# Optimization experiments

Hardware: AMD Instinct MI355X
Metric: run time of the kernel (lower is better)

The kernel has to match this reference:

```python
import jax, jax.numpy as jnp
import numpy as np

H_LSTM = 80          # span-encoder LSTM hidden
SPAN_DIM = 4 * H_LSTM  # 320
ADU_DIM = 256        # han_out_size
HEADS = 3
HAN_HID = 256
CTX_DIM = 200


def lstm(x, W_ih, W_hh, b, reverse=False):
    # x: [T, B, In] -> hidden states [T, B, H]; torch gate order i,f,g,o
    H = W_hh.shape[1]
    B = x.shape[1]

    def step(carry, xt):
        h, c = carry
        z = xt @ W_ih.T + h @ W_hh.T + b
        i, f, g, o = jnp.split(z, 4, axis=-1)
        c = jax.nn.sigmoid(f) * c + jax.nn.sigmoid(i) * jnp.tanh(g)
        h = jax.nn.sigmoid(o) * jnp.tanh(c)
        return (h, c), h

    init = (jnp.zeros((B, H), x.dtype), jnp.zeros((B, H), x.dtype))
    _, hs = jax.lax.scan(step, init, x, reverse=reverse)
    return hs


def span_rep(seq, spans):
    # seq [L, 2H], spans [..., 2] -> [..., 4H]
    f, bwd = seq[:, :H_LSTM], seq[:, H_LSTM:]
    i, j = spans[..., 0], spans[..., 1]
    fi1, fj = f[i - 1], f[j]
    bi, bj1 = bwd[i], bwd[j + 1]
    return jnp.concatenate([fj - fi1, bi - bj1, fi1, bj1], axis=-1)


def gat_metapath(h, src, dst, emask, W, a_l, a_r, bias):
    # single-metapath GATConv (dgl semantics): h [A, Din], W [K, Din, D]
    A = h.shape[0]
    hp = jnp.einsum('ad,kdo->ako', h, W)  # [A,K,D]
    e = jax.nn.leaky_relu(jnp.einsum('eko,ko->ek', hp[src], a_l)
                          + jnp.einsum('eko,ko->ek', hp[dst], a_r), 0.2)
    e = jnp.where(emask[:, None], e, -1e9)
    m = jax.ops.segment_max(e, dst, num_segments=A)           # [A,K]
    ex = jnp.where(emask[:, None], jnp.exp(e - m[dst]), 0.0)
    den = jax.ops.segment_sum(ex, dst, num_segments=A)
    alpha = ex / jnp.maximum(den[dst], 1e-9)                  # edge softmax per dst
    out = jax.ops.segment_sum(alpha[:, :, None] * hp[src], dst, num_segments=A)
    out = jax.nn.elu(out + bias)                              # [A,K,D]
    return out.reshape(A, -1)                                 # [A, K*D]


def attn_pool(feats, vals, mask, W1, b1, W2, b2):
    # tiny MLP -> Softmax over axis 0 over the kept (masked) set
    s = jnp.maximum(feats @ W1 + b1, 0.0) @ W2 + b2           # [N,1]
    s = jnp.where(mask[:, None], s, -1e9)
    a = jnp.where(mask[:, None], jax.nn.softmax(s, axis=0), 0.0)
    out = (a * vals).sum(0)
    return jnp.where(mask.any(), out, jnp.zeros_like(out))


def _forward(token_embed, info_scores,
             Wih_f, Whh_f, b_f, Wih_b, Whh_b, b_b,
             W_gat, a_l, a_r, b_gat, W_sem, b_sem, q_sem, W_pred, b_pred,
             W_adu1, b_adu1, W_adu2, b_adu2,
             W_inn1, b_inn1, W_inn2, b_inn2,
             W_int1, b_int1, W_int2, b_int2,
             Wih_c, Whh_c, b_c,
             comment_spans, adu_spans, adu_masks, local_masks,
             inner_src, inner_dst, inner_rel, inner_mask,
             inter_src, inter_dst, inter_rel, inter_mask):
    # bidirectional span encoder over frozen LF token embeddings
    x = token_embed.transpose(1, 0, 2)                        # [L, C, 768]
    hf = lstm(x, Wih_f, Whh_f, b_f)
    hb = lstm(x, Wih_b, Whh_b, b_b, reverse=True)
    span_enc = jnp.concatenate([hf, hb], -1).transpose(1, 0, 2)  # [C, L, 2H]

    def per_comment(seq, cspan, aspans, amask, lmask,
                    isrc, idst, irel, imask_e,
                    tsrc, tdst, trel, tmask_e, info):
        cemb = span_rep(seq, cspan)                           # [320]
        adus = span_rep(seq, aspans) * amask[:, None]         # [A, 320]
        A = adus.shape[0]
        # meta-paths: inner Attack, inner Support, inter AttackedBy(rev), inter SupportedBy(rev)
        srcs = jnp.stack([isrc, isrc, tdst, tdst])
        dsts = jnp.stack([idst, idst, tsrc, tsrc])
        masks = jnp.stack([imask_e & (irel == 0), imask_e & (irel == 1),
                           tmask_e & (trel == 0), tmask_e & (trel == 1)])
        z = jax.vmap(gat_metapath, in_axes=(None, 0, 0, 0, 0, 0, 0, 0))(
            adus, srcs, dsts, masks, W_gat, a_l, a_r, b_gat)  # [4, A, K*D]
        # semantic attention across meta-paths (masked mean over real nodes)
        w = jnp.tanh(z @ W_sem + b_sem) @ q_sem               # [4, A]
        w = (w * amask[None, :]).sum(1) / jnp.maximum(amask.sum(), 1)
        beta = jax.nn.softmax(w)                              # [4]
        zfin = jnp.einsum('m,mad->ad', beta, z)               # [A, K*D]
        adu_embeds = zfin @ W_pred + b_pred                   # [A, 256]
        # ADU attention pooling over locally-used ADUs
        feats = jnp.concatenate(
            [jnp.broadcast_to(cemb, (A, SPAN_DIM)), adu_embeds], -1)
        attended_adu = attn_pool(feats, adu_embeds, amask & lmask,
                                 W_adu1, b_adu1, W_adu2, b_adu2)

        def pair_attend(se, de, rel, me, W1, b1, W2, b2):
            # relation lut: Attack(0)->[0,1], Support(1)->[1,0]
            onehot = jnp.stack([rel, 1 - rel], -1).astype(adu_embeds.dtype)
            pe = jnp.concatenate([adu_embeds[se], adu_embeds[de], onehot], -1)  # [E,514]
            fp = jnp.concatenate(
                [jnp.broadcast_to(cemb, (pe.shape[0], SPAN_DIM)), pe], -1)
            return attn_pool(fp, pe, me, W1, b1, W2, b2)

        attended_inner = pair_attend(isrc, idst, irel, imask_e,
                                     W_inn1, b_inn1, W_inn2, b_inn2)
        # revert_inter_post_relations=True: embed = cat(emb[pair1], emb[pair0], rel)
        attended_inter = pair_attend(tdst, tsrc, trel, tmask_e,
                                     W_int1, b_int1, W_int2, b_int2)
        return jnp.concatenate([attended_adu, attended_inner, attended_inter,
                                info, cemb])                  # [1608]

    wo_ctx = jax.vmap(per_comment)(span_enc, comment_spans, adu_spans, adu_masks,
                                   local_masks, inner_src, inner_dst, inner_rel,
                                   inner_mask, inter_src, inter_dst, inter_rel,
                                   inter_mask, info_scores)   # [C, 1608]
    # comment compressor LSTM along the comment sequence (batch = 1)
    ctx = lstm(wo_ctx[:, None, :], Wih_c, Whh_c, b_c)[:, 0, :]  # [C, 200]
    return jnp.concatenate([ctx, wo_ctx], -1)                 # [C, 1808]


def setup_inputs():
    C, L, A, E, INFO = 64, 1024, 32, 48, 4
    key = jax.random.key(0)
    ks = iter(jax.random.split(key, 64))
    rng = np.random.default_rng(0)

    def u(shape):  # uniform init as in _weight_init, scaled for stability
        return jax.random.uniform(next(ks), shape, jnp.float32, -0.1, 0.1)

    token_embed = jax.random.normal(next(ks), (C, L, 768), jnp.float32)
    info_scores = jax.random.normal(next(ks), (C, INFO), jnp.float32)
    ci = rng.integers(1, L // 2, C)
    cj = rng.integers(L // 2, L - 2, C)
    comment_spans = jnp.stack([jnp.asarray(ci), jnp.asarray(cj)], 1).astype(jnp.int32)
    ai = rng.integers(1, L - 40, (C, A))
    adu_spans = jnp.stack([jnp.asarray(ai), jnp.asarray(ai + rng.integers(1, 30, (C, A)))], -1).astype(jnp.int32)
    adu_masks = jnp.ones((C, A), jnp.bool_)
    local_masks = jnp.asarray(rng.integers(0, 2, (C, A)) > 0)
    ei = lambda hi, shp: jnp.asarray(rng.integers(0, hi, shp), jnp.int32)
    eb = lambda shp: jnp.asarray(rng.integers(0, 2, shp) > 0)
    inp = dict(token_embed=token_embed, info_scores=info_scores,
               comment_spans=comment_spans, adu_spans=adu_spans,
               adu_masks=adu_masks, local_masks=local_masks,
               inner_src=ei(A, (C, E)), inner_dst=ei(A, (C, E)),
               inner_rel=ei(2, (C, E)), inner_mask=eb((C, E)),
               inter_src=ei(A, (C, E)), inter_dst=ei(A, (C, E)),
               inter_rel=ei(2, (C, E)), inter_mask=eb((C, E)))
    D_WO = SPAN_DIM + ADU_DIM * 5 + 4 + INFO  # 1608
    params = dict(
        Wih_f=u((4 * H_LSTM, 768)), Whh_f=u((4 * H_LSTM, H_LSTM)), b_f=u((4 * H_LSTM,)),
        Wih_b=u((4 * H_LSTM, 768)), Whh_b=u((4 * H_LSTM, H_LSTM)), b_b=u((4 * H_LSTM,)),
        W_gat=u((4, HEADS, SPAN_DIM, HAN_HID)), a_l=u((4, HEADS, HAN_HID)),
        a_r=u((4, HEADS, HAN_HID)), b_gat=u((4, HEADS, HAN_HID)),
        W_sem=u((HEADS * HAN_HID, 128)), b_sem=u((128,)), q_sem=u((128,)),
        W_pred=u((HEADS * HAN_HID, ADU_DIM)), b_pred=u((ADU_DIM,)),
        W_adu1=u((SPAN_DIM + ADU_DIM, 16)), b_adu1=u((16,)), W_adu2=u((16, 1)), b_adu2=u((1,)),
        W_inn1=u((SPAN_DIM + 2 * ADU_DIM + 2, 16)), b_inn1=u((16,)), W_inn2=u((16, 1)), b_inn2=u((1,)),
        W_int1=u((SPAN_DIM + 2 * ADU_DIM + 2, 16)), b_int1=u((16,)), W_int2=u((16, 1)), b_int2=u((1,)),
        Wih_c=u((4 * CTX_DIM, D_WO)), Whh_c=u((4 * CTX_DIM, CTX_DIM)), b_c=u((4 * CTX_DIM,)))
    inp.update(params)
    return inp


def reference(token_embed, info_scores,
              Wih_f, Whh_f, b_f, Wih_b, Whh_b, b_b,
              W_gat, a_l, a_r, b_gat, W_sem, b_sem, q_sem, W_pred, b_pred,
              W_adu1, b_adu1, W_adu2, b_adu2,
              W_inn1, b_inn1, W_inn2, b_inn2,
              W_int1, b_int1, W_int2, b_int2,
              Wih_c, Whh_c, b_c,
              comment_spans, adu_spans, adu_masks, local_masks,
              inner_src, inner_dst, inner_rel, inner_mask,
              inter_src, inter_dst, inter_rel, inter_mask):
    return _forward(token_embed, info_scores,
                    Wih_f, Whh_f, b_f, Wih_b, Whh_b, b_b,
                    W_gat, a_l, a_r, b_gat, W_sem, b_sem, q_sem, W_pred, b_pred,
                    W_adu1, b_adu1, W_adu2, b_adu2,
                    W_inn1, b_inn1, W_inn2, b_inn2,
                    W_int1, b_int1, W_int2, b_int2,
                    Wih_c, Whh_c, b_c,
                    comment_spans, adu_spans, adu_masks, local_masks,
                    inner_src, inner_dst, inner_rel, inner_mask,
                    inter_src, inter_dst, inter_rel, inter_mask)
```

## Files before the change

### kernel.cpp

```cpp
#include <hip/hip_runtime.h>
#include <hip/hip_bf16.h>
#include <hip/hip_fp16.h>
#include <stdint.h>

typedef unsigned int u32;
typedef unsigned short u16;
typedef __attribute__((ext_vector_type(8))) short short8;
typedef __attribute__((ext_vector_type(4))) float f32x4;
typedef _Float16 half2v __attribute__((ext_vector_type(2)));

#if defined(__has_builtin)
#if __has_builtin(__builtin_amdgcn_fdot2)
#define HAVE_FDOT2 1
#endif
#endif

__device__ __forceinline__ float bf2f_u(u32 lo16) { return __uint_as_float(lo16 << 16); }
__device__ __forceinline__ u32 f2bf_bits(float x) {
  u32 u = __float_as_uint(x);
  return (u + 0x7fffu + ((u >> 16) & 1u)) >> 16;
}
__device__ __forceinline__ u32 pk2bf(float x, float y) {
  return f2bf_bits(x) | (f2bf_bits(y) << 16);
}
__device__ __forceinline__ u32 pk2bf_tr(float x, float y) {
  return (__float_as_uint(y) & 0xffff0000u) | (__float_as_uint(x) >> 16);
}
__device__ __forceinline__ u32 pkh(float x, float y) {
  return (u32)__half_as_ushort(__float2half(x)) |
         ((u32)__half_as_ushort(__float2half(y)) << 16);
}
__device__ __forceinline__ float dot2h(u32 w, u32 h, float acc) {
#ifdef HAVE_FDOT2
  return __builtin_amdgcn_fdot2(__builtin_bit_cast(half2v, w), __builtin_bit_cast(half2v, h),
                                acc, false);
#else
  union { u32 u; __half2 h2; } uw, uh;
  uw.u = w; uh.u = h;
  float2 wf = __half22float2(uw.h2);
  float2 hf = __half22float2(uh.h2);
  return acc + wf.x * hf.x + wf.y * hf.y;
#endif
}
__device__ __forceinline__ float sigf(float x) { return 1.0f / (1.0f + __expf(-x)); }
__device__ __forceinline__ float tanhf_fast(float x) {
  float ax = fabsf(x);
  float e = __expf(-2.0f * ax);
  float t = (1.0f - e) / (1.0f + e);
  return x < 0.0f ? -t : t;
}
__device__ __forceinline__ float eluf(float x) { return x > 0.0f ? x : __expf(x) - 1.0f; }
__device__ __forceinline__ float lreluf(float x) { return x > 0.0f ? x : 0.2f * x; }

__device__ __forceinline__ int maskmode(const void* am) { return (*(const u32*)am) > 0xFFu; }
__device__ __forceinline__ int ldmask(const void* p, int i, int mb) {
  return mb ? (int)((const unsigned char*)p)[i] : ((const int*)p)[i];
}

__global__ void k_marker(float* out) { out[0] = 12345.0f; }

__global__ void k_prep(const float* __restrict__ Wgat, const float* __restrict__ al,
                       const float* __restrict__ ar, float* __restrict__ alproj,
                       float* __restrict__ arproj) {
  int idx = blockIdx.x * 256 + threadIdx.x;
  if (idx >= 3840) return;
  int mk = idx / 320, d = idx % 320;
  const float* wrow = Wgat + ((size_t)mk * 320 + d) * 256;
  const float* alp = al + mk * 256;
  const float* arp = ar + mk * 256;
  float sa = 0.f, sb = 0.f;
  for (int o = 0; o < 256; ++o) {
    float w = wrow[o];
    sa += w * alp[o];
    sb += w * arp[o];
  }
  alproj[idx] = sa;
  arproj[idx] = sb;
}

__global__ void k_pack(const float* __restrict__ whhc, uint4* __restrict__ wt4) {
  int idx = blockIdx.x * 256 + threadIdx.x;
  if (idx >= 20000) return;
  int k4 = idx / 800, r = idx % 800;
  const float* p = whhc + r * 200 + k4 * 8;
  wt4[idx] = (uint4){pkh(p[0], p[1]), pkh(p[2], p[3]), pkh(p[4], p[5]), pkh(p[6], p[7])};
}

__global__ __launch_bounds__(256) void k_gemm_in(
    const float* __restrict__ emb, const float* __restrict__ Wf, const float* __restrict__ Wb,
    const float* __restrict__ biasf, const float* __restrict__ biasb, float* __restrict__ Z) {
  __shared__ u16 Albs[128 * 40];
  __shared__ u16 Blbs[128 * 40];
  __shared__ float bias_l[128];
  const int tid = threadIdx.x;
  const int n0 = blockIdx.x * 128;
  const int m0 = blockIdx.y * 128;

  if (tid < 128) {
    int ng = n0 + tid;
    bias_l[tid] = (ng < 320) ? biasf[ng] : biasb[ng - 320];
  }

  const int srow = tid >> 1, shalf = tid & 1;
  const float* asrc = emb + (size_t)(m0 + srow) * 768 + shalf * 16;
  const int ngb = n0 + srow;
  const float* bsrc =
      ((ngb < 320) ? (Wf + (size_t)ngb * 768) : (Wb + (size_t)(ngb - 320) * 768)) + shalf * 16;
  u32* aw = (u32*)&Albs[srow * 40 + shalf * 16];
  u32* bw = (u32*)&Blbs[srow * 40 + shalf * 16];

  const int lane = tid & 63;
  const int lr = lane & 15, sub = lane >> 4;
  const int wv = tid >> 6, wm = wv >> 1, wn = wv & 1;
  const u16* abase = &Albs[(wm * 64 + lr) * 40 + sub * 8];
  const u16* bbase = &Blbs[(wn * 64 + lr) * 40 + sub * 8];

  f32x4 acc[4][4];
#pragma unroll
  for (int i = 0; i < 4; ++i)
#pragma unroll
    for (int j = 0; j < 4; ++j) acc[i][j] = (f32x4)(0.f);

  float4 a0, a1, a2, a3, b0, b1, b2, b3;
  u32 pra[8], prb[8];
  a0 = *(const float4*)(asrc + 0); a1 = *(const float4*)(asrc + 4);
  a2 = *(const float4*)(asrc + 8); a3 = *(const float4*)(asrc + 12);
  b0 = *(const float4*)(bsrc + 0); b1 = *(const float4*)(bsrc + 4);
  b2 = *(const float4*)(bsrc + 8); b3 = *(const float4*)(bsrc + 12);
  pra[0] = pk2bf_tr(a0.x, a0.y); pra[1] = pk2bf_tr(a0.z, a0.w);
  pra[2] = pk2bf_tr(a1.x, a1.y); pra[3] = pk2bf_tr(a1.z, a1.w);
  pra[4] = pk2bf_tr(a2.x, a2.y); pra[5] = pk2bf_tr(a2.z, a2.w);
  pra[6] = pk2bf_tr(a3.x, a3.y); pra[7] = pk2bf_tr(a3.z, a3.w);
  prb[0] = pk2bf_tr(b0.x, b0.y); prb[1] = pk2bf_tr(b0.z, b0.w);
  prb[2] = pk2bf_tr(b1.x, b1.y); prb[3] = pk2bf_tr(b1.z, b1.w);
  prb[4] = pk2bf_tr(b2.x, b2.y); prb[5] = pk2bf_tr(b2.z, b2.w);
  prb[6] = pk2bf_tr(b3.x, b3.y); prb[7] = pk2bf_tr(b3.z, b3.w);

  for (int it = 0; it < 24; ++it) {
    __syncthreads();
#pragma unroll
    for (int q = 0; q < 8; ++q) { aw[q] = pra[q]; bw[q] = prb[q]; }
    __syncthreads();
    const bool more = (it + 1 < 24);
    if (more) {
      const int k0 = (it + 1) * 32;
      a0 = *(const float4*)(asrc + k0); a1 = *(const float4*)(asrc + k0 + 4);
      a2 = *(const float4*)(asrc + k0 + 8); a3 = *(const float4*)(asrc + k0 + 12);
      b0 = *(const float4*)(bsrc + k0); b1 = *(const float4*)(bsrc + k0 + 4);
      b2 = *(const float4*)(bsrc + k0 + 8); b3 = *(const float4*)(bsrc + k0 + 12);
    }
    short8 bfr[4];
#pragma unroll
    for (int nf = 0; nf < 4; ++nf) bfr[nf] = *(const short8*)(bbase + nf * 640);
#pragma unroll
    for (int mf = 0; mf < 4; ++mf) {
      short8 af = *(const short8*)(abase + mf * 640);
#pragma unroll
      for (int nf = 0; nf < 4; ++nf)
        acc[mf][nf] = __builtin_amdgcn_mfma_f32_16x16x32_bf16(af, bfr[nf], acc[mf][nf], 0, 0, 0);
    }
    if (more) {
      pra[0] = pk2bf_tr(a0.x, a0.y); pra[1] = pk2bf_tr(a0.z, a0.w);
      pra[2] = pk2bf_tr(a1.x, a1.y); pra[3] = pk2bf_tr(a1.z, a1.w);
      pra[4] = pk2bf_tr(a2.x, a2.y); pra[5] = pk2bf_tr(a2.z, a2.w);
      pra[6] = pk2bf_tr(a3.x, a3.y); pra[7] = pk2bf_tr(a3.z, a3.w);
      prb[0] = pk2bf_tr(b0.x, b0.y); prb[1] = pk2bf_tr(b0.z, b0.w);
      prb[2] = pk2bf_tr(b1.x, b1.y); prb[3] = pk2bf_tr(b1.z, b1.w);
      prb[4] = pk2bf_tr(b2.x, b2.y); prb[5] = pk2bf_tr(b2.z, b2.w);
      prb[6] = pk2bf_tr(b3.x, b3.y); prb[7] = pk2bf_tr(b3.z, b3.w);
    }
  }

#pragma unroll
  for (int mf = 0; mf < 4; ++mf) {
#pragma unroll
    for (int nf = 0; nf < 4; ++nf) {
      int col = wn * 64 + nf * 16 + lr;
      float bias = bias_l[col];
      size_t mrow = (size_t)m0 + wm * 64 + mf * 16 + sub * 4;
#pragma unroll
      for (int j = 0; j < 4; ++j)
        Z[(mrow + j) * 640 + n0 + col] = acc[mf][nf][j] + bias;
    }
  }
}

__global__ __launch_bounds__(320, 1) void k_lstm_tok(const float* __restrict__ Z,
                                                     const float* __restrict__ Whhf,
                                                     const float* __restrict__ Whhb,
                                                     float* __restrict__ hf,
                                                     float* __restrict__ hb) {
  __shared__ uint2 wq[20 * 320];
  __shared__ alignas(16) u32 hpk[40];
  __shared__ float zbuf[320];
  const int tid = threadIdx.x;
  const int c = blockIdx.x >> 1;
  const int dir = blockIdx.x & 1;
  const float* Whh = dir ? Whhb : Whhf;
  float* hout = dir ? hb : hf;

  for (int idx = tid; idx < 20 * 320; idx += 320) {
    int k4 = idx / 320, r = idx % 320;
    const float* p = Whh + (size_t)r * 80 + k4 * 4;
    wq[idx] = (uint2){pkh(p[0], p[1]), pkh(p[2], p[3])};
  }
  if (tid < 40) hpk[tid] = 0;
  __syncthreads();

  const int j = tid;
  const uint2* wcol = wq + j;
  uint2 wv0 = wcol[0], wv1 = wcol[320], wv2 = wcol[640], wv3 = wcol[960];
  uint2 wv4 = wcol[1280], wv5 = wcol[1600], wv6 = wcol[1920], wv7 = wcol[2240];
  uint2 wv8 = wcol[2560], wv9 = wcol[2880], wv10 = wcol[3200], wv11 = wcol[3520];
  uint2 wv12 = wcol[3840], wv13 = wcol[4160], wv14 = wcol[4480], wv15 = wcol[4800];
  uint2 wv16 = wcol[5120], wv17 = wcol[5440], wv18 = wcol[5760], wv19 = wcol[6080];
  asm volatile("" : "+v"(wv0.x), "+v"(wv0.y), "+v"(wv1.x), "+v"(wv1.y), "+v"(wv2.x),
                    "+v"(wv2.y), "+v"(wv3.x), "+v"(wv3.y), "+v"(wv4.x), "+v"(wv4.y),
                    "+v"(wv5.x), "+v"(wv5.y), "+v"(wv6.x), "+v"(wv6.y), "+v"(wv7.x),
                    "+v"(wv7.y), "+v"(wv8.x), "+v"(wv8.y), "+v"(wv9.x), "+v"(wv9.y));
  asm volatile("" : "+v"(wv10.x), "+v"(wv10.y), "+v"(wv11.x), "+v"(wv11.y), "+v"(wv12.x),
                    "+v"(wv12.y), "+v"(wv13.x), "+v"(wv13.y), "+v"(wv14.x), "+v"(wv14.y),
                    "+v"(wv15.x), "+v"(wv15.y), "+v"(wv16.x), "+v"(wv16.y), "+v"(wv17.x),
                    "+v"(wv17.y), "+v"(wv18.x), "+v"(wv18.y), "+v"(wv19.x), "+v"(wv19.y));

  const int sgn = dir ? -1 : 1;
  const int t0 = dir ? 1023 : 0;
  const float* zb = Z + (size_t)c * 1024 * 640 + dir * 320 + j;
  float zc = zb[(size_t)t0 * 640];
  float zn = zb[(size_t)(t0 + sgn) * 640];
  float cst = 0.f;

  for (int t = 0; t < 1024; ++t) {
    const int tt = t0 + sgn * t;
    float zp = 0.f;
    if (t + 2 < 1024) zp = zb[(size_t)(t0 + sgn * (t + 2)) * 640];
    float a0 = zc, a1 = 0.f, a2 = 0.f, a3 = 0.f;
    {
      uint4 h0 = *(const uint4*)&hpk[0];
      a0 = dot2h(wv0.x, h0.x, a0); a1 = dot2h(wv0.y, h0.y, a1);
      a2 = dot2h(wv1.x, h0.z, a2); a3 = dot2h(wv1.y, h0.w, a3);
      uint4 h1 = *(const uint4*)&hpk[4];
      a0 = dot2h(wv2.x, h1.x, a0); a1 = dot2h(wv2.y, h1.y, a1);
      a2 = dot2h(wv3.x, h1.z, a2); a3 = dot2h(wv3.y, h1.w, a3);
      uint4 h2 = *(const uint4*)&hpk[8];
      a0 = dot2h(wv4.x, h2.x, a0); a1 = dot2h(wv4.y, h2.y, a1);
      a2 = dot2h(wv5.x, h2.z, a2); a3 = dot2h(wv5.y, h2.w, a3);
      uint4 h3 = *(const uint4*)&hpk[12];
      a0 = dot2h(wv6.x, h3.x, a0); a1 = dot2h(wv6.y, h3.y, a1);
      a2 = dot2h(wv7.x, h3.z, a2); a3 = dot2h(wv7.y, h3.w, a3);
      uint4 h4 = *(const uint4*)&hpk[16];
      a0 = dot2h(wv8.x, h4.x, a0); a1 = dot2h(wv8.y, h4.y, a1);
      a2 = dot2h(wv9.x, h4.z, a2); a3 = dot2h(wv9.y, h4.w, a3);
      uint4 h5 = *(const uint4*)&hpk[20];
      a0 = dot2h(wv10.x, h5.x, a0); a1 = dot2h(wv10.y, h5.y, a1);
      a2 = dot2h(wv11.x, h5.z, a2); a3 = dot2h(wv11.y, h5.w, a3);
      uint4 h6 = *(const uint4*)&hpk[24];
      a0 = dot2h(wv12.x, h6.x, a0); a1 = dot2h(wv12.y, h6.y, a1);
      a2 = dot2h(wv13.x, h6.z, a2); a3 = dot2h(wv13.y, h6.w, a3);
      uint4 h7 = *(const uint4*)&hpk[28];
      a0 = dot2h(wv14.x, h7.x, a0); a1 = dot2h(wv14.y, h7.y, a1);
      a2 = dot2h(wv15.x, h7.z, a2); a3 = dot2h(wv15.y, h7.w, a3);
      uint4 h8 = *(const uint4*)&hpk[32];
      a0 = dot2h(wv16.x, h8.x, a0); a1 = dot2h(wv16.y, h8.y, a1);
      a2 = dot2h(wv17.x, h8.z, a2); a3 = dot2h(wv17.y, h8.w, a3);
      uint4 h9 = *(const uint4*)&hpk[36];
      a0 = dot2h(wv18.x, h9.x, a0); a1 = dot2h(wv18.y, h9.y, a1);
      a2 = dot2h(wv19.x, h9.z, a2); a3 = dot2h(wv19.y, h9.w, a3);
    }
    zbuf[j] = (a0 + a1) + (a2 + a3);
    __syncthreads();
    if (j < 80) {
      float iv = sigf(zbuf[j]);
      float fv = sigf(zbuf[80 + j]);
      float gv = tanhf_fast(zbuf[160 + j]);
      float ov = sigf(zbuf[240 + j]);
      cst = fv * cst + iv * gv;
      float h = ov * tanhf_fast(cst);
      ((u16*)hpk)[j] = __half_as_ushort(__float2half(h));
      hout[((size_t)c * 1024 + tt) * 80 + j] = h;
    }
    zc = zn; zn = zp;
    __syncthreads();
  }
}

__device__ __forceinline__ float span_val(const float* __restrict__ hf,
                                          const float* __restrict__ hb, int c, int i, int j,
                                          int d) {
  size_t base = (size_t)c * 1024 * 80;
  if (d < 80) return hf[base + (size_t)j * 80 + d] - hf[base + (size_t)(i - 1) * 80 + d];
  if (d < 160) return hb[base + (size_t)i * 80 + (d - 80)] - hb[base + (size_t)(j + 1) * 80 + (d - 80)];
  if (d < 240) return hf[base + (size_t)(i - 1) * 80 + (d - 160)];
  return hb[base + (size_t)(j + 1) * 80 + (d - 240)];
}

__global__ __launch_bounds__(256) void k_span(const float* __restrict__ hf,
                                              const float* __restrict__ hb,
                                              const int* __restrict__ cspan,
                                              const int* __restrict__ aspan,
                                              const void* __restrict__ amask,
                                              float* __restrict__ adus, float* __restrict__ cembo) {
  const int c = blockIdx.x, tid = threadIdx.x;
  const int mb = maskmode(amask);
  int ci = cspan[c * 2], cj = cspan[c * 2 + 1];
  for (int d = tid; d < 320; d += 256) cembo[c * 320 + d] = span_val(hf, hb, c, ci, cj, d);
  for (int idx = tid; idx < 32 * 320; idx += 256) {
    int a = idx / 320, d = idx % 320;
    float v = 0.f;
    if (ldmask(amask, c * 32 + a, mb)) {
      int ai = aspan[(c * 32 + a) * 2], aj = aspan[(c * 32 + a) * 2 + 1];
      v = span_val(hf, hb, c, ai, aj, d);
    }
    adus[(size_t)c * 10240 + idx] = v;
  }
}

__global__ __launch_bounds__(256) void k_gat(
    const float* __restrict__ adus_ws, const float* __restrict__ alproj,
    const float* __restrict__ arproj, const float* __restrict__ Wgat,
    const float* __restrict__ bgat, const int* __restrict__ isrc, const int* __restrict__ idst,
    const int* __restrict__ irel, const void* __restrict__ imask, const int* __restrict__ tsrc,
    const int* __restrict__ tdst, const int* __restrict__ trel, const void* __restrict__ tmask,
    const void* __restrict__ amdet, float* __restrict__ zgat) {
  __shared__ float adus_l[32][321];
  __shared__ float Wst[16][64];
  __shared__ float hp_t[32][66];
  __shared__ float sl_l[96], sr_l[96];
  __shared__ float e_l[144], alpha_l[144], mx_l[96], den_l[96];
  __shared__ int src_l[48], dst_l[48], valid_l[48];
  const int c = blockIdx.x >> 2, m = blockIdx.x & 3;
  const int tid = threadIdx.x;
  const int mb = maskmode(amdet);

  if (tid < 48) {
    int e = tid, s, d, r, mk;
    if (m < 2) {
      s = isrc[c * 48 + e]; d = idst[c * 48 + e]; r = irel[c * 48 + e];
      mk = ldmask(imask, c * 48 + e, mb);
    } else {
      s = tdst[c * 48 + e]; d = tsrc[c * 48 + e]; r = trel[c * 48 + e];
      mk = ldmask(tmask, c * 48 + e, mb);
    }
    src_l[e] = s; dst_l[e] = d; valid_l[e] = (mk != 0) && (r == (m & 1));
  }
  for (int idx = tid; idx < 32 * 320; idx += 256)
    adus_l[idx / 320][idx % 320] = adus_ws[(size_t)c * 10240 + idx];
  __syncthreads();

  if (tid < 96) {
    int a = tid & 31, k = tid >> 5;
    const float* alp = alproj + (m * 3 + k) * 320;
    const float* arp = arproj + (m * 3 + k) * 320;
    float sa = 0.f, sb = 0.f;
    for (int d = 0; d < 320; ++d) {
      float v = adus_l[a][d];
      sa += v * alp[d];
      sb += v * arp[d];
    }
    sl_l[a * 3 + k] = sa;
    sr_l[a * 3 + k] = sb;
  }
  __syncthreads();
  if (tid < 144) {
    int e = tid % 48, k = tid / 48;
    float v = -1e30f;
    if (valid_l[e]) v = lreluf(sl_l[src_l[e] * 3 + k] + sr_l[dst_l[e] * 3 + k]);
    e_l[e * 3 + k] = v;
  }
  __syncthreads();
  if (tid < 96) {
    int a = tid & 31, k = tid >> 5;
    float mx = -1e30f;
    for (int e = 0; e < 48; ++e)
      if (valid_l[e] && dst_l[e] == a) mx = fmaxf(mx, e_l[e * 3 + k]);
    float den = 0.f;
    for (int e = 0; e < 48; ++e)
      if (valid_l[e] && dst_l[e] == a) den += __expf(e_l[e * 3 + k] - mx);
    mx_l[a * 3 + k] = mx;
    den_l[a * 3 + k] = den;
  }
  __syncthreads();
  if (tid < 144) {
    int e = tid % 48, k = tid / 48;
    float v = 0.f;
    if (valid_l[e]) {
      int d = dst_l[e];
      v = __expf(e_l[e * 3 + k] - mx_l[d * 3 + k]) / fmaxf(den_l[d * 3 + k], 1e-9f);
    }
    alpha_l[e * 3 + k] = v;
  }
  __syncthreads();

  const int ag = tid >> 3, og = tid & 7;
  for (int k = 0; k < 3; ++k) {
    for (int ot = 0; ot < 4; ++ot) {
      float acc[8];
#pragma unroll
      for (int i = 0; i < 8; ++i) acc[i] = 0.f;
      for (int dt = 0; dt < 320; dt += 16) {
        {
          int dd = tid >> 4, oq = (tid & 15) * 4;
          const float* p = Wgat + ((size_t)((m * 3 + k) * 320 + dt + dd)) * 256 + ot * 64 + oq;
          float4 v = *(const float4*)p;
          Wst[dd][oq + 0] = v.x;
          Wst[dd][oq + 1] = v.y;
          Wst[dd][oq + 2] = v.z;
          Wst[dd][oq + 3] = v.w;
        }
        __syncthreads();
#pragma unroll
        for (int dd = 0; dd < 16; ++dd) {
          float av = adus_l[ag][dt + dd];
          const float4 w0 = *(const float4*)(&Wst[dd][og * 8]);
          const float4 w1 = *(const float4*)(&Wst[dd][og * 8 + 4]);
          acc[0] += av * w0.x; acc[1] += av * w0.y; acc[2] += av * w0.z; acc[3] += av * w0.w;
          acc[4] += av * w1.x; acc[5] += av * w1.y; acc[6] += av * w1.z; acc[7] += av * w1.w;
        }
        __syncthreads();
      }
#pragma unroll
      for (int i = 0; i < 8; ++i) hp_t[ag][og * 8 + i] = acc[i];
      __syncthreads();
      float oacc[8];
#pragma unroll
      for (int i = 0; i < 8; ++i) oacc[i] = 0.f;
      for (int e = 0; e < 48; ++e) {
        if (valid_l[e] && dst_l[e] == ag) {
          float alv = alpha_l[e * 3 + k];
          int s = src_l[e];
#pragma unroll
          for (int i = 0; i < 8; ++i) oacc[i] += alv * hp_t[s][og * 8 + i];
        }
      }
#pragma unroll
      for (int i = 0; i < 8; ++i) {
        int o = ot * 64 + og * 8 + i;
        float v = eluf(oacc[i] + bgat[(m * 3 + k) * 256 + o]);
        zgat[((size_t)(c * 4 + m) * 32 + ag) * 768 + k * 256 + o] = v;
      }
      __syncthreads();
    }
  }
}

__global__ __launch_bounds__(256) void k_sem(const float* __restrict__ zgat,
                                             const float* __restrict__ Wsem,
                                             const float* __restrict__ bsem,
                                             const float* __restrict__ qsem,
                                             const void* __restrict__ amask,
                                             float* __restrict__ wsem) {
  __shared__ float Wst[64][128];
  __shared__ float zl[32][64];
  __shared__ float wred[256];
  __shared__ float war[32];
  const int c = blockIdx.x >> 2, m = blockIdx.x & 3;
  const int tid = threadIdx.x;
  const int mb = maskmode(amask);
  const int a = tid >> 3, hg = tid & 7;
  float acc[16];
#pragma unroll
  for (int i = 0; i < 16; ++i) acc[i] = 0.f;
  const float* zbase = zgat + (size_t)(c * 4 + m) * 32 * 768;
  for (int jt = 0; jt < 768; jt += 64) {
    for (int l = 0; l < 8; ++l) {
      int f4 = l * 256 + tid;
      int row = f4 >> 5, c4 = (f4 & 31) * 4;
      *(float4*)&Wst[row][c4] = *(const float4*)(Wsem + (size_t)(jt + row) * 128 + c4);
    }
    for (int l = 0; l < 2; ++l) {
      int f4 = l * 256 + tid;
      int row = f4 >> 4, c4 = (f4 & 15) * 4;
      *(float4*)&zl[row][c4] = *(const float4*)(zbase + (size_t)row * 768 + jt + c4);
    }
    __syncthreads();
    for (int j = 0; j < 64; ++j) {
      float zv = zl[a][j];
      const float* wp = &Wst[j][hg * 16];
#pragma unroll
      for (int i = 0; i < 16; ++i) acc[i] += zv * wp[i];
    }
    __syncthreads();
  }
  float wp_ = 0.f;
#pragma unroll
  for (int i = 0; i < 16; ++i) {
    int h = hg * 16 + i;
    wp_ += tanhf_fast(acc[i] + bsem[h]) * qsem[h];
  }
  wred[tid] = wp_;
  __syncthreads();
  if (tid < 32) {
    float s = 0.f;
    for (int q = 0; q < 8; ++q) s += wred[tid * 8 + q];
    war[tid] = s;
  }
  __syncthreads();
  if (tid == 0) {
    float s = 0.f;
    int cnt = 0;
    for (int aa = 0; aa < 32; ++aa)
      if (ldmask(amask, c * 32 + aa, mb)) { s += war[aa]; cnt++; }
    wsem[c * 4 + m] = s / (float)(cnt > 1 ? cnt : 1);
  }
}

__global__ __launch_bounds__(256) void k_comment(
    const float* __restrict__ zgat, const float* __restrict__ wsem,
    const float* __restrict__ cemb_ws, const float* __restrict__ Wpred,
    const float* __restrict__ bpred, const float* __restrict__ Wadu1,
    const float* __restrict__ badu1, const float* __restrict__ Wadu2,
    const float* __restrict__ badu2, const float* __restrict__ Winn1,
    const float* __restrict__ binn1, const float* __restrict__ Winn2,
    const float* __restrict__ binn2, const float* __restrict__ Wint1,
    const float* __restrict__ bint1, const float* __restrict__ Wint2,
    const float* __restrict__ bint2, const float* __restrict__ info,
    const void* __restrict__ amask, const void* __restrict__ lmask,
    const int* __restrict__ isrc, const int* __restrict__ idst,
    const int* __restrict__ irel, const void* __restrict__ imask, const int* __restrict__ tsrc,
    const int* __restrict__ tdst, const int* __restrict__ trel, const void* __restrict__ tmask,
    float* __restrict__ woctx, float* __restrict__ dout) {
  __shared__ float zf[32][133];
  __shared__ float ae[32][257];
  __shared__ float cemb_l[320];
  __shared__ float beta_l[4];
  __shared__ float pred_l[48][16];
  __shared__ float sE[48], alE[48];
  __shared__ int seL[48], deL[48], relL[48], mskL[48];
  __shared__ float wredA[256];
  __shared__ float sA[32], alA[32];
  __shared__ int mskA[32];
  const int c = blockIdx.x, tid = threadIdx.x;
  const int mb = maskmode(amask);

  if (tid == 0) {
    float w0 = wsem[c * 4], w1 = wsem[c * 4 + 1], w2 = wsem[c * 4 + 2], w3 = wsem[c * 4 + 3];
    float mx = fmaxf(fmaxf(w0, w1), fmaxf(w2, w3));
    float e0 = __expf(w0 - mx), e1 = __expf(w1 - mx), e2 = __expf(w2 - mx), e3 = __expf(w3 - mx);
    float s = e0 + e1 + e2 + e3;
    beta_l[0] = e0 / s; beta_l[1] = e1 / s; beta_l[2] = e2 / s; beta_l[3] = e3 / s;
  }
  for (int d = tid; d < 320; d += 256) cemb_l[d] = cemb_ws[c * 320 + d];
  __syncthreads();

  const int ag = tid >> 5;
  const int og = tid & 31;
  float acc[4][8];
#pragma unroll
  for (int i = 0; i < 4; ++i)
#pragma unroll
    for (int j = 0; j < 8; ++j) acc[i][j] = 0.f;
  const float b0 = beta_l[0], b1 = beta_l[1], b2 = beta_l[2], b3 = beta_l[3];
  const float* zc0 = zgat + (size_t)(c * 4 + 0) * 32 * 768;
  const float* zc1 = zgat + (size_t)(c * 4 + 1) * 32 * 768;
  const float* zc2 = zgat + (size_t)(c * 4 + 2) * 32 * 768;
  const float* zc3 = zgat + (size_t)(c * 4 + 3) * 32 * 768;
  for (int jt = 0; jt < 768; jt += 128) {
    for (int l = 0; l < 16; ++l) {
      int idx = l * 256 + tid;
      int a = idx >> 7, j = idx & 127;
      size_t off = (size_t)a * 768 + jt + j;
      zf[a][j] = b0 * zc0[off] + b1 * zc1[off] + b2 * zc2[off] + b3 * zc3[off];
    }
    __syncthreads();
    for (int j = 0; j < 128; ++j) {
      const float* wp = Wpred + (size_t)(jt + j) * 256 + og * 8;
      float4 w0v = *(const float4*)wp;
      float4 w1v = *(const float4*)(wp + 4);
      float w8[8] = {w0v.x, w0v.y, w0v.z, w0v.w, w1v.x, w1v.y, w1v.z, w1v.w};
      float z0 = zf[ag * 4 + 0][j], z1 = zf[ag * 4 + 1][j];
      float z2 = zf[ag * 4 + 2][j], z3 = zf[ag * 4 + 3][j];
#pragma unroll
      for (int jj = 0; jj < 8; ++jj) {
        acc[0][jj] += z0 * w8[jj];
        acc[1][jj] += z1 * w8[jj];
        acc[2][jj] += z2 * w8[jj];
        acc[3][jj] += z3 * w8[jj];
      }
    }
    __syncthreads();
  }
#pragma unroll
  for (int i = 0; i < 4; ++i)
#pragma unroll
    for (int jj = 0; jj < 8; ++jj)
      ae[ag * 4 + i][og * 8 + jj] = acc[i][jj] + bpred[og * 8 + jj];
  __syncthreads();

  {
    const int a = tid >> 3, hg = tid & 7;
    float sacc = 0.f;
    for (int hh = 0; hh < 2; ++hh) {
      int h = hg * 2 + hh;
      float d = badu1[h];
      for (int dd = 0; dd < 320; ++dd) d += cemb_l[dd] * Wadu1[dd * 16 + h];
      for (int dd = 0; dd < 256; ++dd) d += ae[a][dd] * Wadu1[(320 + dd) * 16 + h];
      sacc += fmaxf(d, 0.f) * Wadu2[h];
    }
    wredA[tid] = sacc;
  }
  __syncthreads();
  if (tid < 32) {
    float s = badu2[0];
    for (int q = 0; q < 8; ++q) s += wredA[tid * 8 + q];
    sA[tid] = s;
    mskA[tid] = (ldmask(amask, c * 32 + tid, mb) != 0) && (ldmask(lmask, c * 32 + tid, mb) != 0);
  }
  __syncthreads();
  if (tid == 0) {
    float mx = -1e30f;
    int any = 0;
    for (int a = 0; a < 32; ++a)
      if (mskA[a]) { any = 1; mx = fmaxf(mx, sA[a]); }
    float s = 0.f;
    for (int a = 0; a < 32; ++a) {
      float v = mskA[a] ? __expf(sA[a] - mx) : 0.f;
      alA[a] = v;
      s += v;
    }
    if (any)
      for (int a = 0; a < 32; ++a) alA[a] /= s;
  }
  __syncthreads();
  {
    int o = tid;
    float v = 0.f;
    for (int a = 0; a < 32; ++a) v += alA[a] * ae[a][o];
    woctx[c * 1608 + o] = v;
    dout[(size_t)c * 1808 + 200 + o] = v;
  }
  __syncthreads();

  for (int pp = 0; pp < 2; ++pp) {
    const float *W1, *b1v, *W2, *b2v;
    const int *seP, *deP, *relP;
    const void* mskP;
    int outoff;
    if (pp == 0) {
      W1 = Winn1; b1v = binn1; W2 = Winn2; b2v = binn2;
      seP = isrc; deP = idst; relP = irel; mskP = imask; outoff = 256;
    } else {
      W1 = Wint1; b1v = bint1; W2 = Wint2; b2v = bint2;
      seP = tdst; deP = tsrc; relP = trel; mskP = tmask; outoff = 770;
    }
    if (tid < 48) {
      seL[tid] = seP[c * 48 + tid];
      deL[tid] = deP[c * 48 + tid];
      relL[tid] = relP[c * 48 + tid];
      mskL[tid] = (ldmask(mskP, c * 48 + tid, mb) != 0);
    }
    __syncthreads();
    for (int u = tid; u < 768; u += 256) {
      int e = u >> 4, h = u & 15;
      int se = seL[e], de = deL[e];
      float rel = (float)relL[e];
      float d = b1v[h];
      for (int dd = 0; dd < 320; ++dd) d += cemb_l[dd] * W1[dd * 16 + h];
      for (int dd = 0; dd < 256; ++dd) d += ae[se][dd] * W1[(320 + dd) * 16 + h];
      for (int dd = 0; dd < 256; ++dd) d += ae[de][dd] * W1[(576 + dd) * 16 + h];
      d += rel * W1[832 * 16 + h] + (1.f - rel) * W1[833 * 16 + h];
      pred_l[e][h] = fmaxf(d, 0.f) * W2[h];
    }
    __syncthreads();
    if (tid < 48) {
      float s = b2v[0];
      for (int h = 0; h < 16; ++h) s += pred_l[tid][h];
      sE[tid] = s;
    }
    __syncthreads();
    if (tid == 0) {
      float mx = -1e30f;
      int any = 0;
      for (int e = 0; e < 48; ++e)
        if (mskL[e]) { any = 1; mx = fmaxf(mx, sE[e]); }
      float s = 0.f;
      for (int e = 0; e < 48; ++e) {
        float v = mskL[e] ? __expf(sE[e] - mx) : 0.f;
        alE[e] = v;
        s += v;
      }
      if (any)
        for (int e = 0; e < 48; ++e) alE[e] /= s;
    }
    __syncthreads();
    for (int dim = tid; dim < 514; dim += 256) {
      float v = 0.f;
      for (int e = 0; e < 48; ++e) {
        float alv = alE[e];
        float pe;
        if (dim < 256) pe = ae[seL[e]][dim];
        else if (dim < 512) pe = ae[deL[e]][dim - 256];
        else if (dim == 512) pe = (float)relL[e];
        else pe = 1.f - (float)relL[e];
        v += alv * pe;
      }
      woctx[c * 1608 + outoff + dim] = v;
      dout[(size_t)c * 1808 + 200 + outoff + dim] = v;
    }
    __syncthreads();
  }

  if (tid < 4) {
    float v = info[c * 4 + tid];
    woctx[c * 1608 + 1284 + tid] = v;
    dout[(size_t)c * 1808 + 200 + 1284 + tid] = v;
  }
  for (int d = tid; d < 320; d += 256) {
    float v = cemb_l[d];
    woctx[c * 1608 + 1288 + d] = v;
    dout[(size_t)c * 1808 + 200 + 1288 + d] = v;
  }
}

__global__ __launch_bounds__(256) void k_ctx_in(const float* __restrict__ woctx,
                                                const float* __restrict__ Wihc,
                                                const float* __restrict__ bc,
                                                float* __restrict__ xc) {
  __shared__ float woc[64][133];
  __shared__ float Wst[8][128];
  const int r0 = blockIdx.x * 8;
  const int tid = threadIdx.x;
  const int t = tid & 63, rg = tid >> 6;
  float a0 = 0.f, a1 = 0.f;
  for (int d0 = 0; d0 < 1608; d0 += 128) {
    int jn = 1608 - d0;
    if (jn > 128) jn = 128;
    for (int l = 0; l < 32; ++l) {
      int idx = l * 256 + tid;
      int tt = idx >> 7, j = idx & 127;
      woc[tt][j] = (j < jn) ? woctx[(size_t)tt * 1608 + d0 + j] : 0.f;
    }
    {
      int rr = tid >> 5, jb = tid & 31;
      for (int q = 0; q < 4; ++q) {
        int jj = jb * 4 + q;
        Wst[rr][jj] = (jj < jn) ? Wihc[(size_t)(r0 + rr) * 1608 + d0 + jj] : 0.f;
      }
    }
    __syncthreads();
    for (int j = 0; j < 128; ++j) {
      float x = woc[t][j];
      a0 += x * Wst[rg * 2 + 0][j];
      a1 += x * Wst[rg * 2 + 1][j];
    }
    __syncthreads();
  }
  int r = r0 + rg * 2;
  xc[t * 800 + r] = a0 + bc[r];
  xc[t * 800 + r + 1] = a1 + bc[r + 1];
}

__global__ __launch_bounds__(832) void k_ctx_rec(const float* __restrict__ xc,
                                                 const uint4* __restrict__ wt4,
                                                 float* __restrict__ dout) {
  __shared__ alignas(16) u32 hl2[100];
  __shared__ float zc[800];
  const int tid = threadIdx.x;
  if (tid < 100) hl2[tid] = 0;
  float cst = 0.f;
  __syncthreads();
  for (int t = 0; t < 64; ++t) {
    if (tid < 800) {
      float a0 = xc[t * 800 + tid], a1 = 0.f, a2 = 0.f, a3 = 0.f;
#pragma unroll 5
      for (int k4 = 0; k4 < 25; ++k4) {
        uint4 wv = wt4[(size_t)k4 * 800 + tid];
        uint4 hq = *(const uint4*)&hl2[k4 * 4];
        a0 = dot2h(wv.x, hq.x, a0);
        a1 = dot2h(wv.y, hq.y, a1);
        a2 = dot2h(wv.z, hq.z, a2);
        a3 = dot2h(wv.w, hq.w, a3);
      }
      zc[tid] = (a0 + a1) + (a2 + a3);
    }
    __syncthreads();
    if (tid < 200) {
      float iv = sigf(zc[tid]);
      float fv = sigf(zc[200 + tid]);
      float gv = tanhf_fast(zc[400 + tid]);
      float ov = sigf(zc[600 + tid]);
      cst = fv * cst + iv * gv;
      float h = ov * tanhf_fast(cst);
      ((u16*)hl2)[tid] = __half_as_ushort(__float2half(h));
      dout[(size_t)t * 1808 + tid] = h;
    }
    __syncthreads();
  }
}

extern "C" void kernel_launch(void* const* d_in, const int* in_sizes, int n_in, void* d_out,
                              int out_size, void* d_ws, size_t ws_size, hipStream_t stream) {
  const float* emb = (const float*)d_in[0];
  const float* info = (const float*)d_in[1];
  const int* cspan = (const int*)d_in[2];
  const int* aspan = (const int*)d_in[3];
  const void* amask = d_in[4];
  const void* lmask = d_in[5];
  const int* isrc = (const int*)d_in[6];
  const int* idst = (const int*)d_in[7];
  const int* irel = (const int*)d_in[8];
  const void* imask = d_in[9];
  const int* tsrc = (const int*)d_in[10];
  const int* tdst = (const int*)d_in[11];
  const int* trel = (const int*)d_in[12];
  const void* tmask = d_in[13];
  const float* Wihf = (const float*)d_in[14];
  const float* Whhf = (const float*)d_in[15];
  const float* bfv = (const float*)d_in[16];
  const float* Wihb = (const float*)d_in[17];
  const float* Whhb = (const float*)d_in[18];
  const float* bbv = (const float*)d_in[19];
  const float* Wgat = (const float*)d_in[20];
  const float* al = (const float*)d_in[21];
  const float* ar = (const float*)d_in[22];
  const float* bgat = (const float*)d_in[23];
  const float* Wsem = (const float*)d_in[24];
  const float* bsem = (const float*)d_in[25];
  const float* qsem = (const float*)d_in[26];
  const float* Wpred = (const float*)d_in[27];
  const float* bpred = (const float*)d_in[28];
  const float* Wadu1 = (const float*)d_in[29];
  const float* badu1 = (const float*)d_in[30];
  const float* Wadu2 = (const float*)d_in[31];
  const float* badu2 = (const float*)d_in[32];
  const float* Winn1 = (const float*)d_in[33];
  const float* binn1 = (const float*)d_in[34];
  const float* Winn2 = (const float*)d_in[35];
  const float* binn2 = (const float*)d_in[36];
  const float* Wint1 = (const float*)d_in[37];
  const float* bint1 = (const float*)d_in[38];
  const float* Wint2 = (const float*)d_in[39];
  const float* bint2 = (const float*)d_in[40];
  const float* Wihc = (const float*)d_in[41];
  const float* Whhc = (const float*)d_in[42];
  const float* bc = (const float*)d_in[43];
  float* out = (float*)d_out;
  float* ws = (float*)d_ws;

  const size_t OFF_Z = 0;
  const size_t OFF_HF = OFF_Z + (size_t)65536 * 640;
  const size_t OFF_HB = OFF_HF + (size_t)64 * 1024 * 80;
  const size_t OFF_ZG = OFF_HB + (size_t)64 * 1024 * 80;
  const size_t OFF_AD = OFF_ZG + (size_t)64 * 4 * 32 * 768;
  const size_t OFF_CE = OFF_AD + (size_t)64 * 32 * 320;
  const size_t OFF_WS4 = OFF_CE + 64 * 320;
  const size_t OFF_ALP = OFF_WS4 + 256;
  const size_t OFF_ARP = OFF_ALP + 3840;
  const size_t OFF_WO = OFF_ARP + 3840;
  const size_t OFF_XC = OFF_WO + (size_t)64 * 1608;
  const size_t OFF_WT = OFF_XC + (size_t)64 * 800;
  const size_t TOTAL = OFF_WT + 80000;

  if (n_in < 44 || ws_size < TOTAL * sizeof(float)) {
    k_marker<<<1, 1, 0, stream>>>(out);
    return;
  }

  k_prep<<<15, 256, 0, stream>>>(Wgat, al, ar, ws + OFF_ALP, ws + OFF_ARP);
  k_pack<<<79, 256, 0, stream>>>(Whhc, (uint4*)(ws + OFF_WT));
  dim3 g1(5, 512);
  k_gemm_in<<<g1, 256, 0, stream>>>(emb, Wihf, Wihb, bfv, bbv, ws + OFF_Z);
  k_lstm_tok<<<128, 320, 0, stream>>>(ws + OFF_Z, Whhf, Whhb, ws + OFF_HF, ws + OFF_HB);
  k_span<<<64, 256, 0, stream>>>(ws + OFF_HF, ws + OFF_HB, cspan, aspan, amask, ws + OFF_AD,
                                 ws + OFF_CE);
  k_gat<<<256, 256, 0, stream>>>(ws + OFF_AD, ws + OFF_ALP, ws + OFF_ARP, Wgat, bgat, isrc, idst,
                                 irel, imask, tsrc, tdst, trel, tmask, amask, ws + OFF_ZG);
  k_sem<<<256, 256, 0, stream>>>(ws + OFF_ZG, Wsem, bsem, qsem, amask, ws + OFF_WS4);
  k_comment<<<64, 256, 0, stream>>>(ws + OFF_ZG, ws + OFF_WS4, ws + OFF_CE, Wpred, bpred, Wadu1,
                                    badu1, Wadu2, badu2, Winn1, binn1, Winn2, binn2, Wint1, bint1,
                                    Wint2, bint2, info, amask, lmask, isrc, idst, irel, imask,
                                    tsrc, tdst, trel, tmask, ws + OFF_WO, out);
  k_ctx_in<<<100, 256, 0, stream>>>(ws + OFF_WO, Wihc, bc, ws + OFF_XC);
  k_ctx_rec<<<1, 832, 0, stream>>>(ws + OFF_XC, (const uint4*)(ws + OFF_WT), out);
}
```

Baseline: 1.849 ms.

## Parallelize GAT projection prep, prefetch weight tiles, stage MLP weights in LDS

k_prep now uses one wavefront per output row with a shuffle reduction instead of a serial 256-long loop per thread. The GAT and comment kernels prefetch the next weight tile or row into registers to hide global load latency. The ADU and pair MLP weights are copied into a large shared buffer so the strided inner loops read LDS instead of global memory. The asm register pins on the LSTM weights are removed, which may change register allocation in the recurrence kernel; the added LDS use also lowers occupancy of k_comment.

```diff
diff --git a/kernel.cpp b/kernel.cpp
--- a/kernel.cpp
+++ b/kernel.cpp
@@ -19,9 +19,6 @@
 __device__ __forceinline__ u32 f2bf_bits(float x) {
   u32 u = __float_as_uint(x);
   return (u + 0x7fffu + ((u >> 16) & 1u)) >> 16;
-}
-__device__ __forceinline__ u32 pk2bf(float x, float y) {
-  return f2bf_bits(x) | (f2bf_bits(y) << 16);
 }
 __device__ __forceinline__ u32 pk2bf_tr(float x, float y) {
   return (__float_as_uint(y) & 0xffff0000u) | (__float_as_uint(x) >> 16);
@@ -59,23 +56,32 @@
 
 __global__ void k_marker(float* out) { out[0] = 12345.0f; }
 
-__global__ void k_prep(const float* __restrict__ Wgat, const float* __restrict__ al,
-                       const float* __restrict__ ar, float* __restrict__ alproj,
-                       float* __restrict__ arproj) {
-  int idx = blockIdx.x * 256 + threadIdx.x;
-  if (idx >= 3840) return;
-  int mk = idx / 320, d = idx % 320;
+__global__ __launch_bounds__(256) void k_prep(const float* __restrict__ Wgat,
+                                              const float* __restrict__ al,
+                                              const float* __restrict__ ar,
+                                              float* __restrict__ alproj,
+                                              float* __restrict__ arproj) {
+  int w = blockIdx.x * 4 + (threadIdx.x >> 6);
+  int lane = threadIdx.x & 63;
+  if (w >= 3840) return;
+  int mk = w / 320, d = w % 320;
   const float* wrow = Wgat + ((size_t)mk * 320 + d) * 256;
   const float* alp = al + mk * 256;
   const float* arp = ar + mk * 256;
   float sa = 0.f, sb = 0.f;
-  for (int o = 0; o < 256; ++o) {
-    float w = wrow[o];
-    sa += w * alp[o];
-    sb += w * arp[o];
-  }
-  alproj[idx] = sa;
-  arproj[idx] = sb;
+#pragma unroll
+  for (int q = 0; q < 4; ++q) {
+    int o = lane + q * 64;
+    float wv = wrow[o];
+    sa += wv * alp[o];
+    sb += wv * arp[o];
+  }
+#pragma unroll
+  for (int off = 32; off; off >>= 1) {
+    sa += __shfl_down(sa, off, 64);
+    sb += __shfl_down(sb, off, 64);
+  }
+  if (lane == 0) { alproj[w] = sa; arproj[w] = sb; }
 }
 
 __global__ void k_pack(const float* __restrict__ whhc, uint4* __restrict__ wt4) {
@@ -100,7 +106,6 @@
     int ng = n0 + tid;
     bias_l[tid] = (ng < 320) ? biasf[ng] : biasb[ng - 320];
   }
-
   const int srow = tid >> 1, shalf = tid & 1;
   const float* asrc = emb + (size_t)(m0 + srow) * 768 + shalf * 16;
   const int ngb = n0 + srow;
@@ -170,7 +175,6 @@
       prb[6] = pk2bf_tr(b3.x, b3.y); prb[7] = pk2bf_tr(b3.z, b3.w);
     }
   }
-
 #pragma unroll
   for (int mf = 0; mf < 4; ++mf) {
 #pragma unroll
@@ -214,14 +218,6 @@
   uint2 wv8 = wcol[2560], wv9 = wcol[2880], wv10 = wcol[3200], wv11 = wcol[3520];
   uint2 wv12 = wcol[3840], wv13 = wcol[4160], wv14 = wcol[4480], wv15 = wcol[4800];
   uint2 wv16 = wcol[5120], wv17 = wcol[5440], wv18 = wcol[5760], wv19 = wcol[6080];
-  asm volatile("" : "+v"(wv0.x), "+v"(wv0.y), "+v"(wv1.x), "+v"(wv1.y), "+v"(wv2.x),
-                    "+v"(wv2.y), "+v"(wv3.x), "+v"(wv3.y), "+v"(wv4.x), "+v"(wv4.y),
-                    "+v"(wv5.x), "+v"(wv5.y), "+v"(wv6.x), "+v"(wv6.y), "+v"(wv7.x),
-                    "+v"(wv7.y), "+v"(wv8.x), "+v"(wv8.y), "+v"(wv9.x), "+v"(wv9.y));
-  asm volatile("" : "+v"(wv10.x), "+v"(wv10.y), "+v"(wv11.x), "+v"(wv11.y), "+v"(wv12.x),
-                    "+v"(wv12.y), "+v"(wv13.x), "+v"(wv13.y), "+v"(wv14.x), "+v"(wv14.y),
-                    "+v"(wv15.x), "+v"(wv15.y), "+v"(wv16.x), "+v"(wv16.y), "+v"(wv17.x),
-                    "+v"(wv17.y), "+v"(wv18.x), "+v"(wv18.y), "+v"(wv19.x), "+v"(wv19.y));
 
   const int sgn = dir ? -1 : 1;
   const int t0 = dir ? 1023 : 0;
@@ -276,7 +272,7 @@
       float ov = sigf(zbuf[240 + j]);
       cst = fv * cst + iv * gv;
       float h = ov * tanhf_fast(cst);
-      ((u16*)hpk)[j] = __half_as_ushort(__float2half(h));
+      ((u16*)hpk)[j] = (u16)__half_as_ushort(__float2half(h));
       hout[((size_t)c * 1024 + tt) * 80 + j] = h;
     }
     zc = zn; zn = zp;
@@ -392,22 +388,22 @@
   __syncthreads();
 
   const int ag = tid >> 3, og = tid & 7;
+  const int dd_ = tid >> 4, oq_ = (tid & 15) * 4;
   for (int k = 0; k < 3; ++k) {
     for (int ot = 0; ot < 4; ++ot) {
       float acc[8];
 #pragma unroll
       for (int i = 0; i < 8; ++i) acc[i] = 0.f;
+      float4 pref = *(const float4*)(Wgat + ((size_t)((m * 3 + k) * 320 + dd_)) * 256 + ot * 64 + oq_);
       for (int dt = 0; dt < 320; dt += 16) {
-        {
-          int dd = tid >> 4, oq = (tid & 15) * 4;
-          const float* p = Wgat + ((size_t)((m * 3 + k) * 320 + dt + dd)) * 256 + ot * 64 + oq;
-          float4 v = *(const float4*)p;
-          Wst[dd][oq + 0] = v.x;
-          Wst[dd][oq + 1] = v.y;
-          Wst[dd][oq + 2] = v.z;
-          Wst[dd][oq + 3] = v.w;
-        }
+        Wst[dd_][oq_ + 0] = pref.x;
+        Wst[dd_][oq_ + 1] = pref.y;
+        Wst[dd_][oq_ + 2] = pref.z;
+        Wst[dd_][oq_ + 3] = pref.w;
         __syncthreads();
+        if (dt + 16 < 320)
+          pref = *(const float4*)(Wgat +
+                                  ((size_t)((m * 3 + k) * 320 + dt + 16 + dd_)) * 256 + ot * 64 + oq_);
 #pragma unroll
         for (int dd = 0; dd < 16; ++dd) {
           float av = adus_l[ag][dt + dd];
@@ -521,6 +517,7 @@
     float* __restrict__ woctx, float* __restrict__ dout) {
   __shared__ float zf[32][133];
   __shared__ float ae[32][257];
+  __shared__ float wbuf[13344];
   __shared__ float cemb_l[320];
   __shared__ float beta_l[4];
   __shared__ float pred_l[48][16];
@@ -562,10 +559,16 @@
       zf[a][j] = b0 * zc0[off] + b1 * zc1[off] + b2 * zc2[off] + b3 * zc3[off];
     }
     __syncthreads();
+    const float* wp0 = Wpred + (size_t)jt * 256 + og * 8;
+    float4 w0v = *(const float4*)wp0;
+    float4 w1v = *(const float4*)(wp0 + 4);
     for (int j = 0; j < 128; ++j) {
-      const float* wp = Wpred + (size_t)(jt + j) * 256 + og * 8;
-      float4 w0v = *(const float4*)wp;
-      float4 w1v = *(const float4*)(wp + 4);
+      float4 n0v, n1v;
+      if (j + 1 < 128) {
+        const float* wp = Wpred + (size_t)(jt + j + 1) * 256 + og * 8;
+        n0v = *(const float4*)wp;
+        n1v = *(const float4*)(wp + 4);
+      }
       float w8[8] = {w0v.x, w0v.y, w0v.z, w0v.w, w1v.x, w1v.y, w1v.z, w1v.w};
       float z0 = zf[ag * 4 + 0][j], z1 = zf[ag * 4 + 1][j];
       float z2 = zf[ag * 4 + 2][j], z3 = zf[ag * 4 + 3][j];
@@ -576,6 +579,7 @@
         acc[2][jj] += z2 * w8[jj];
         acc[3][jj] += z3 * w8[jj];
       }
+      if (j + 1 < 128) { w0v = n0v; w1v = n1v; }
     }
     __syncthreads();
   }
@@ -584,6 +588,7 @@
 #pragma unroll
     for (int jj = 0; jj < 8; ++jj)
       ae[ag * 4 + i][og * 8 + jj] = acc[i][jj] + bpred[og * 8 + jj];
+  for (int idx = tid; idx < 9216; idx += 256) wbuf[idx] = Wadu1[idx];
   __syncthreads();
 
   {
@@ -592,8 +597,8 @@
     for (int hh = 0; hh < 2; ++hh) {
       int h = hg * 2 + hh;
       float d = badu1[h];
-      for (int dd = 0; dd < 320; ++dd) d += cemb_l[dd] * Wadu1[dd * 16 + h];
-      for (int dd = 0; dd < 256; ++dd) d += ae[a][dd] * Wadu1[(320 + dd) * 16 + h];
+      for (int dd = 0; dd < 320; ++dd) d += cemb_l[dd] * wbuf[dd * 16 + h];
+      for (int dd = 0; dd < 256; ++dd) d += ae[a][dd] * wbuf[(320 + dd) * 16 + h];
       sacc += fmaxf(d, 0.f) * Wadu2[h];
     }
     wredA[tid] = sacc;
@@ -648,16 +653,17 @@
       relL[tid] = relP[c * 48 + tid];
       mskL[tid] = (ldmask(mskP, c * 48 + tid, mb) != 0);
     }
+    for (int idx = tid; idx < 13344; idx += 256) wbuf[idx] = W1[idx];
     __syncthreads();
     for (int u = tid; u < 768; u += 256) {
       int e = u >> 4, h = u & 15;
       int se = seL[e], de = deL[e];
       float rel = (float)relL[e];
       float d = b1v[h];
-      for (int dd = 0; dd < 320; ++dd) d += cemb_l[dd] * W1[dd * 16 + h];
-      for (int dd = 0; dd < 256; ++dd) d += ae[se][dd] * W1[(320 + dd) * 16 + h];
-      for (int dd = 0; dd < 256; ++dd) d += ae[de][dd] * W1[(576 + dd) * 16 + h];
-      d += rel * W1[832 * 16 + h] + (1.f - rel) * W1[833 * 16 + h];
+      for (int dd = 0; dd < 320; ++dd) d += cemb_l[dd] * wbuf[dd * 16 + h];
+      for (int dd = 0; dd < 256; ++dd) d += ae[se][dd] * wbuf[(320 + dd) * 16 + h];
+      for (int dd = 0; dd < 256; ++dd) d += ae[de][dd] * wbuf[(576 + dd) * 16 + h];
+      d += rel * wbuf[832 * 16 + h] + (1.f - rel) * wbuf[833 * 16 + h];
       pred_l[e][h] = fmaxf(d, 0.f) * W2[h];
     }
     __syncthreads();
@@ -855,7 +861,7 @@
     return;
   }
 
-  k_prep<<<15, 256, 0, stream>>>(Wgat, al, ar, ws + OFF_ALP, ws + OFF_ARP);
+  k_prep<<<960, 256, 0, stream>>>(Wgat, al, ar, ws + OFF_ALP, ws + OFF_ARP);
   k_pack<<<79, 256, 0, stream>>>(Whhc, (uint4*)(ws + OFF_WT));
   dim3 g1(5, 512);
   k_gemm_in<<<g1, 256, 0, stream>>>(emb, Wihf, Wihb, bfv, bbv, ws + OFF_Z);
```

New measurement: 1.683 ms (median of 2 runs). 9.0% less time.
